# Kernel optimization log

Measured on AMD Instinct MI355X. Metric: run time of the kernel, lower is better.

Reference implementation:

```python
import jax, jax.numpy as jnp
import numpy as np

H, W, S, B = 256, 256, 16, 8  # dim=(H,W); S hardcoded in forward; B = 1 + events[-1,-1]
N = 4_000_000


def _shift2d(a, dy, dx):
    """Replicates F.pad(a, (pad(dx) + pad(dy)))[:H,:W] where pad(n)=(n,0) if n>=0 else (0,-n).
    Positive diff shifts content right/down and zero-fills; negative diff is a no-op
    (right/bottom padding followed by top-left crop is identity)."""
    sy = jnp.maximum(dy, 0)
    sx = jnp.maximum(dx, 0)
    a = jnp.roll(a, shift=(sy, sx), axis=(0, 1))
    row = jnp.arange(a.shape[0])[:, None]
    col = jnp.arange(a.shape[1])[None, :]
    return jnp.where((row >= sy) & (col >= sx), a, 0.0)


def setup_inputs():
    key = jax.random.key(0)
    k1, k2, k3, k4 = jax.random.split(key, 4)
    x = jax.random.randint(k1, (N,), 0, W).astype(jnp.float32)
    y = jax.random.randint(k2, (N,), 0, H).astype(jnp.float32)
    t = jax.random.uniform(k3, (N,), minval=1e-3, maxval=1.0)
    p = (jax.random.randint(k4, (N,), 0, 2) * 2 - 1).astype(jnp.float32)
    b = jnp.repeat(jnp.arange(B, dtype=jnp.float32), N // B)  # sorted so events[-1,-1]==B-1
    events = jnp.stack([x, y, t, p, b], axis=1)
    return {"events": events}


def _forward(events):
    x = events[:, 0]
    y = events[:, 1]
    t = events[:, 2]
    bi = events[:, 4].astype(jnp.int32)

    # per-batch time normalization: t /= max(t) within each sample
    t_max = jax.ops.segment_max(t, bi, num_segments=B)
    t = t / t_max[bi]

    xi = x.astype(jnp.int32)
    yi = y.astype(jnp.int32)

    # container: per-pixel event count histogram, (B,H,W)
    idx_c = xi + W * yi + W * H * bi
    container = jnp.zeros(B * H * W, jnp.int32).at[idx_c].add(1).reshape(B, H, W)

    # time_segment[e] = number of thresholds i/S (i=1..S-1) with t >= i/S
    thr = jnp.arange(1, S, dtype=t.dtype) / S
    ts = jnp.searchsorted(thr, t, side='right').astype(jnp.int32)

    # combiner accumulates the segment index itself (as in the torch code)
    idx_cb = xi + W * yi + W * H * ts + W * H * S * bi
    combiner = jnp.zeros(B * S * H * W, jnp.int32).at[idx_cb].add(ts)
    combiner = combiner.reshape(B, S, H, W).astype(jnp.float32)

    # per-(batch, segment) event counts and x/y centroids
    seg = bi * S + ts
    cnt = jax.ops.segment_sum(jnp.ones_like(t), seg, num_segments=B * S).reshape(B, S)
    xm = jax.ops.segment_sum(x, seg, num_segments=B * S).reshape(B, S) / cnt
    ym = jax.ops.segment_sum(y, seg, num_segments=B * S).reshape(B, S) / cnt

    # mean-shift alignment + accumulation of the S segment images
    combined = []
    for b_ in range(B):
        segment = combiner[b_, 0]
        x_mean = xm[b_, 0]
        y_mean = ym[b_, 0]
        pts = cnt[b_, 0]  # note: never updated in the original code
        for i in range(1, S):
            cond = cnt[b_, i] > pts
            tmp = jnp.where(cond, segment, combiner[b_, i])
            base = jnp.where(cond, combiner[b_, i], segment)
            dx = jnp.floor(jnp.where(cond, xm[b_, i] - x_mean, x_mean - xm[b_, i])).astype(jnp.int32)
            dy = jnp.floor(jnp.where(cond, ym[b_, i] - y_mean, y_mean - ym[b_, i])).astype(jnp.int32)
            x_mean = jnp.where(cond, xm[b_, i], x_mean)
            y_mean = jnp.where(cond, ym[b_, i], y_mean)
            segment = base + _shift2d(tmp, dy, dx)
        combined.append(jax.nn.relu(segment - S))
    combined_img = jnp.stack(combined)  # (B,H,W)

    # half-resolution count + mean-timestamp voxel grids
    hw4 = (H // 2) * (W // 2)
    idx_ct = xi // 2 + (W // 2) * (yi // 2) + (W * H * bi) // 4
    counter = jnp.zeros(B * hw4, jnp.int32).at[idx_ct].add(1).astype(jnp.float32)
    divider = jnp.where(counter == 0, 1.0, counter)
    timer = jnp.zeros(B * hw4, jnp.float32).at[idx_ct].add(t) / divider
    counter = counter.reshape(B, H // 2, W // 2)
    timer = timer.reshape(B, H // 2, W // 2)

    # 2x2 difference pooling of the count image
    dyv = container[:, ::2] - container[:, 1::2]
    dyv = (dyv[:, :, ::2] + dyv[:, :, 1::2]).astype(jnp.float32)
    dxv = container[:, :, ::2] - container[:, :, 1::2]
    dxv = (dxv[:, 1::2] + dxv[:, ::2]).astype(jnp.float32)

    # F.interpolate(scale_factor=0.5, mode='nearest') == ::2 subsampling for even H,W
    combined_half = combined_img[:, ::2, ::2]

    return jnp.stack([dxv, dyv, timer, counter, combined_half], axis=1)  # (B,5,H/2,W/2)


def reference(events):
    return _forward(events)
```

## Files before the change

### kernel.cpp

```cpp
#include <hip/hip_runtime.h>

#define SS 16
#define BB 8
#define CHUNKS 32

#define OFF_CNT    0
#define OFF_XS     512
#define OFF_YS     1024
#define OFF_BMAX   1536
#define OFF_P4REP  5632
#define OFF_CMREP  (5632 + 16777216)
#define OFF_XYREC  (5632 + 16777216 + 4194304)
#define OFF_TARR   (5632 + 16777216 + 4194304 + 8000000)
#define OFF_TSREC  (5632 + 16777216 + 4194304 + 8000000 + 16000000)


__global__ void k_prep(const float4* __restrict__ ev4, int nq, unsigned* __restrict__ bmax,
                       uint2* __restrict__ xyrec, float4* __restrict__ tarr,
                       int* __restrict__ cnt, int* __restrict__ xs, int* __restrict__ ys) {
    if (blockIdx.x == 0 && threadIdx.x < BB * SS) {
        cnt[threadIdx.x] = 0; xs[threadIdx.x] = 0; ys[threadIdx.x] = 0;
    }
    int bb = blockIdx.x >> 7;
    long base = (long)bb * nq;
    unsigned m = 0;
    for (int q = (blockIdx.x & 127) * blockDim.x + threadIdx.x; q < nq; q += 128 * blockDim.x) {
        const float4* p = ev4 + (base + q) * 5;
        float4 f0 = p[0], f1 = p[1], f2 = p[2], f3 = p[3], f4 = p[4];
        unsigned xy0 = (unsigned)(int)f0.x | ((unsigned)(int)f0.y << 8)
                     | ((unsigned)(int)f1.y << 16) | ((unsigned)(int)f1.z << 24);
        unsigned xy1 = (unsigned)(int)f2.z | ((unsigned)(int)f2.w << 8)
                     | ((unsigned)(int)f3.w << 16) | ((unsigned)(int)f4.x << 24);
        xyrec[base + q] = make_uint2(xy0, xy1);
        tarr[base + q]  = make_float4(f0.z, f1.w, f3.x, f4.y);
        unsigned t0 = __float_as_uint(f0.z), t1 = __float_as_uint(f1.w);
        unsigned t2 = __float_as_uint(f3.x), t3 = __float_as_uint(f4.y);
        unsigned a = t0 > t1 ? t0 : t1;
        unsigned b2 = t2 > t3 ? t2 : t3;
        a = a > b2 ? a : b2;
        m = m > a ? m : a;
    }
    #pragma unroll
    for (int off = 32; off; off >>= 1) {
        unsigned o = (unsigned)__shfl_xor((int)m, off, 64);
        m = m > o ? m : o;
    }
    __shared__ unsigned sm;
    if (threadIdx.x == 0) sm = 0;
    __syncthreads();
    if ((threadIdx.x & 63) == 0) atomicMax(&sm, m);
    __syncthreads();
    if (threadIdx.x == 0) bmax[blockIdx.x] = sm;
}

__global__ void __launch_bounds__(1024, 8)
k_main(const uint2* __restrict__ xyrec, const float4* __restrict__ tarr, int nq,
       const unsigned* __restrict__ bmax,
       unsigned* __restrict__ p4rep, unsigned short* __restrict__ tsrec,
       int* __restrict__ cnt, int* __restrict__ xs, int* __restrict__ ys) {
    __shared__ unsigned p4s[16384];
    __shared__ unsigned long long stat[SS * 16];
    __shared__ unsigned stmax;
    int bb = blockIdx.x >> 5;
    int ch = blockIdx.x & 31;
    if (threadIdx.x == 0) stmax = 0u;
    if (threadIdx.x < SS * 16) stat[threadIdx.x] = 0ull;
    {
        uint4 z = make_uint4(0u, 0u, 0u, 0u);
        uint4* p4 = (uint4*)p4s;
        for (int i = threadIdx.x; i < 4096; i += 1024) p4[i] = z;
    }
    __syncthreads();
    if (threadIdx.x < 128) atomicMax(&stmax, bmax[bb * 128 + threadIdx.x]);
    __syncthreads();
    float tm = __uint_as_float(stmax);
    long base = (long)bb * nq;
    int slot = threadIdx.x & 15;
    for (int q = ch * 1024 + threadIdx.x; q < nq; q += CHUNKS * 1024) {
        uint2 xy = xyrec[base + q];
        float4 t4 = tarr[base + q];
        float T[4] = { t4.x, t4.y, t4.z, t4.w };
        unsigned XY[4] = { xy.x & 0xFFFFu, xy.x >> 16, xy.y & 0xFFFFu, xy.y >> 16 };
        unsigned tsn = 0;
        #pragma unroll
        for (int k = 0; k < 4; k++) {
            int xi = (int)(XY[k] & 255u), yi = (int)(XY[k] >> 8);
            float tn = __fdiv_rn(T[k], tm);
            int ts = (int)(tn * 16.0f);
            if (ts > 15) ts = 15;
            unsigned qfix = __float2uint_rn(tn * 256.0f);
            unsigned v = qfix | (1u << 14)
                | (((unsigned)(xi & 1) ^ 1u) << 20)
                | (((unsigned)(yi & 1) ^ 1u) << 26);
            atomicAdd(&p4s[((yi >> 1) << 7) + (xi >> 1)], v);
            atomicAdd(&stat[ts * 16 + slot], 1ull | ((unsigned long long)xi << 20)
                                                  | ((unsigned long long)yi << 42));
            tsn |= (unsigned)ts << (4 * k);
        }
        tsrec[base + q] = (unsigned short)tsn;
    }
    __syncthreads();
    {
        uint4* src = (uint4*)p4s;
        uint4* dst = (uint4*)(p4rep + (long)blockIdx.x * 16384);
        for (int i = threadIdx.x; i < 4096; i += 1024) dst[i] = src[i];
    }
    if (threadIdx.x < SS) {
        unsigned long long v = 0ull;
        #pragma unroll
        for (int s = 0; s < 16; s++) v += stat[threadIdx.x * 16 + s];
        if (v) {
            int g = bb * SS + threadIdx.x;
            atomicAdd(&cnt[g], (int)(v & 0xFFFFF));
            atomicAdd(&xs[g],  (int)((v >> 20) & 0x3FFFFF));
            atomicAdd(&ys[g],  (int)(v >> 42));
        }
    }
}

__global__ void __launch_bounds__(1024, 8)
k_comb(const uint2* __restrict__ xyrec, const unsigned short* __restrict__ tsrec, int nq,
       const int* __restrict__ cnt, const int* __restrict__ xs, const int* __restrict__ ys,
       const unsigned* __restrict__ p4rep,
       unsigned* __restrict__ cmrep32, float* __restrict__ out) {
    __shared__ int combs[16384];
    __shared__ double xm[SS], ym[SS];
    __shared__ int cs[SS], ssy[SS], ssx[SS];
    int bb = blockIdx.x >> 5;
    int ch = blockIdx.x & 31;
    {
        int4 z = make_int4(0, 0, 0, 0);
        int4* cb = (int4*)combs;
        for (int i = threadIdx.x; i < 4096; i += 1024) cb[i] = z;
    }
    if (threadIdx.x < SS) {
        int g = bb * SS + threadIdx.x;
        int cc = cnt[g];
        cs[threadIdx.x] = cc;
        xm[threadIdx.x] = (double)xs[g] / (double)cc;
        ym[threadIdx.x] = (double)ys[g] / (double)cc;
    }
    __syncthreads();
    if (threadIdx.x == 0) {
        double x_mean = xm[0], y_mean = ym[0];
        int c0 = cs[0];
        int sy[SS], sx[SS];
        for (int k = 0; k < SS; k++) { sy[k] = 0; sx[k] = 0; }
        for (int k = 1; k < SS; k++) {
            bool cond = cs[k] > c0;
            double ddx = cond ? (xm[k] - x_mean) : (x_mean - xm[k]);
            double ddy = cond ? (ym[k] - y_mean) : (y_mean - ym[k]);
            int dx = (int)floor(ddx);
            int dy = (int)floor(ddy);
            int px = dx > 0 ? dx : 0;
            int py = dy > 0 ? dy : 0;
            if (cond) {
                for (int j = 0; j < k; j++) { sy[j] += py; sx[j] += px; }
                x_mean = xm[k]; y_mean = ym[k];
            } else {
                sy[k] = py; sx[k] = px;
            }
        }
        for (int k = 0; k < SS; k++) { ssy[k] = sy[k]; ssx[k] = sx[k]; }
    }
    __syncthreads();
    long base = (long)bb * nq;
    for (int q = ch * 1024 + threadIdx.x; q < nq; q += CHUNKS * 1024) {
        uint2 xy = xyrec[base + q];
        unsigned tsn = tsrec[base + q];
        unsigned XY[4] = { xy.x & 0xFFFFu, xy.x >> 16, xy.y & 0xFFFFu, xy.y >> 16 };
        #pragma unroll
        for (int k = 0; k < 4; k++) {
            int ts = (int)((tsn >> (4 * k)) & 15u);
            if (ts) {
                int yy = (int)(XY[k] >> 8) + ssy[ts];
                int xx = (int)(XY[k] & 255u) + ssx[ts];
                if (yy < 256 && xx < 256 && !((yy | xx) & 1))
                    atomicAdd(&combs[((yy >> 1) << 7) + (xx >> 1)], ts);
            }
        }
    }
    __syncthreads();
    {
        unsigned* dst = cmrep32 + (long)blockIdx.x * 4096;
        int4* cb = (int4*)combs;
        for (int i = threadIdx.x; i < 4096; i += 1024) {
            int4 c = cb[i];
            dst[i] = (unsigned)c.x | ((unsigned)c.y << 8)
                   | ((unsigned)c.z << 16) | ((unsigned)c.w << 24);
        }
    }
    if (threadIdx.x < 512) {
        int lin = blockIdx.x * 512 + threadIdx.x;
        int hp = lin & 16383;
        int b  = lin >> 14;
        long rb = (long)b * CHUNKS * 16384 + hp;
        unsigned tfix = 0; int c = 0, Ex = 0, Ey = 0;
        #pragma unroll 8
        for (int r = 0; r < CHUNKS; r++) {
            unsigned v = p4rep[rb + (long)r * 16384];
            tfix += v & 0x3FFFu;
            c    += (int)((v >> 14) & 63u);
            Ex   += (int)((v >> 20) & 63u);
            Ey   += (int)(v >> 26);
        }
        float tsum = (float)tfix * (1.0f / 256.0f);
        float ctr = (float)c;
        int obase = (b * 5) << 14;
        out[obase             + hp] = (float)(2 * Ex - c);
        out[obase +     16384 + hp] = (float)(2 * Ey - c);
        out[obase + 2 * 16384 + hp] = tsum / (c == 0 ? 1.0f : ctr);
        out[obase + 3 * 16384 + hp] = ctr;
    }
}

__global__ void k_out(const unsigned* __restrict__ cmrep32, float* __restrict__ out) {
    int lin4 = blockIdx.x * blockDim.x + threadIdx.x;
    int hp4 = lin4 & 4095;
    int b   = lin4 >> 12;
    long rb = (long)b * CHUNKS * 4096 + hp4;
    unsigned accA = 0, accB = 0;
    #pragma unroll 8
    for (int r = 0; r < CHUNKS; r++) {
        unsigned v = cmrep32[rb + (long)r * 4096];
        accA += v & 0x00FF00FFu;
        accB += (v >> 8) & 0x00FF00FFu;
    }
    float c0 = (float)(accA & 0xFFFFu) - 16.0f;
    float c1 = (float)(accB & 0xFFFFu) - 16.0f;
    float c2 = (float)(accA >> 16) - 16.0f;
    float c3 = (float)(accB >> 16) - 16.0f;
    float4 o;
    o.x = c0 < 0.0f ? 0.0f : c0;
    o.y = c1 < 0.0f ? 0.0f : c1;
    o.z = c2 < 0.0f ? 0.0f : c2;
    o.w = c3 < 0.0f ? 0.0f : c3;
    ((float4*)out)[(((b * 5 + 4) << 14) >> 2) + hp4] = o;
}

extern "C" void kernel_launch(void* const* d_in, const int* in_sizes, int n_in,
                              void* d_out, int out_size, void* d_ws, size_t ws_size,
                              hipStream_t stream) {
    const float4* ev4 = (const float4*)d_in[0];
    int n  = in_sizes[0] / 5;
    int nb = n / BB;
    int nq = nb / 4;
    char* ws = (char*)d_ws;
    int*      cnt     = (int*)     (ws + OFF_CNT);
    int*      xs      = (int*)     (ws + OFF_XS);
    int*      ys      = (int*)     (ws + OFF_YS);
    unsigned* bmax    = (unsigned*)(ws + OFF_BMAX);
    unsigned* p4rep   = (unsigned*)(ws + OFF_P4REP);
    unsigned* cmrep32 = (unsigned*)(ws + OFF_CMREP);
    uint2*    xyrec   = (uint2*)   (ws + OFF_XYREC);
    float4*   tarr    = (float4*)  (ws + OFF_TARR);
    unsigned short* tsrec = (unsigned short*)(ws + OFF_TSREC);

    hipLaunchKernelGGL(k_prep, dim3(1024), dim3(256),  0, stream, ev4, nq, bmax,
                       xyrec, tarr, cnt, xs, ys);
    hipLaunchKernelGGL(k_main, dim3(256),  dim3(1024), 0, stream, xyrec, tarr, nq,
                       bmax, p4rep, tsrec, cnt, xs, ys);
    hipLaunchKernelGGL(k_comb, dim3(256),  dim3(1024), 0, stream, xyrec, tsrec, nq,
                       cnt, xs, ys, p4rep, cmrep32, (float*)d_out);
    hipLaunchKernelGGL(k_out,  dim3(32),   dim3(1024), 0, stream,
                       cmrep32, (float*)d_out);
}
```

Baseline: 138.4 us.

## Drop compacted intermediate arrays and re-read raw events in each pass

```diff
diff --git a/kernel.cpp b/kernel.cpp
--- a/kernel.cpp
+++ b/kernel.cpp
@@ -8,15 +8,11 @@
 #define OFF_XS     512
 #define OFF_YS     1024
 #define OFF_BMAX   1536
-#define OFF_P4REP  5632
-#define OFF_CMREP  (5632 + 16777216)
-#define OFF_XYREC  (5632 + 16777216 + 4194304)
-#define OFF_TARR   (5632 + 16777216 + 4194304 + 8000000)
-#define OFF_TSREC  (5632 + 16777216 + 4194304 + 8000000 + 16000000)
-
-
-__global__ void k_prep(const float4* __restrict__ ev4, int nq, unsigned* __restrict__ bmax,
-                       uint2* __restrict__ xyrec, float4* __restrict__ tarr,
+#define OFF_P4REP  8192
+#define OFF_CMREP  (8192 + 16777216)
+
+
+__global__ void k_tmax(const float4* __restrict__ ev4, int nq, unsigned* __restrict__ bmax,
                        int* __restrict__ cnt, int* __restrict__ xs, int* __restrict__ ys) {
     if (blockIdx.x == 0 && threadIdx.x < BB * SS) {
         cnt[threadIdx.x] = 0; xs[threadIdx.x] = 0; ys[threadIdx.x] = 0;
@@ -26,13 +22,7 @@
     unsigned m = 0;
     for (int q = (blockIdx.x & 127) * blockDim.x + threadIdx.x; q < nq; q += 128 * blockDim.x) {
         const float4* p = ev4 + (base + q) * 5;
-        float4 f0 = p[0], f1 = p[1], f2 = p[2], f3 = p[3], f4 = p[4];
-        unsigned xy0 = (unsigned)(int)f0.x | ((unsigned)(int)f0.y << 8)
-                     | ((unsigned)(int)f1.y << 16) | ((unsigned)(int)f1.z << 24);
-        unsigned xy1 = (unsigned)(int)f2.z | ((unsigned)(int)f2.w << 8)
-                     | ((unsigned)(int)f3.w << 16) | ((unsigned)(int)f4.x << 24);
-        xyrec[base + q] = make_uint2(xy0, xy1);
-        tarr[base + q]  = make_float4(f0.z, f1.w, f3.x, f4.y);
+        float4 f0 = p[0], f1 = p[1], f3 = p[3], f4 = p[4];
         unsigned t0 = __float_as_uint(f0.z), t1 = __float_as_uint(f1.w);
         unsigned t2 = __float_as_uint(f3.x), t3 = __float_as_uint(f4.y);
         unsigned a = t0 > t1 ? t0 : t1;
@@ -54,9 +44,8 @@
 }
 
 __global__ void __launch_bounds__(1024, 8)
-k_main(const uint2* __restrict__ xyrec, const float4* __restrict__ tarr, int nq,
-       const unsigned* __restrict__ bmax,
-       unsigned* __restrict__ p4rep, unsigned short* __restrict__ tsrec,
+k_main(const float4* __restrict__ ev4, int nq, const unsigned* __restrict__ bmax,
+       unsigned* __restrict__ p4rep,
        int* __restrict__ cnt, int* __restrict__ xs, int* __restrict__ ys) {
     __shared__ unsigned p4s[16384];
     __shared__ unsigned long long stat[SS * 16];
@@ -77,14 +66,14 @@
     long base = (long)bb * nq;
     int slot = threadIdx.x & 15;
     for (int q = ch * 1024 + threadIdx.x; q < nq; q += CHUNKS * 1024) {
-        uint2 xy = xyrec[base + q];
-        float4 t4 = tarr[base + q];
-        float T[4] = { t4.x, t4.y, t4.z, t4.w };
-        unsigned XY[4] = { xy.x & 0xFFFFu, xy.x >> 16, xy.y & 0xFFFFu, xy.y >> 16 };
-        unsigned tsn = 0;
+        const float4* p = ev4 + (base + q) * 5;
+        float4 f0 = p[0], f1 = p[1], f2 = p[2], f3 = p[3], f4 = p[4];
+        int X[4] = { (int)f0.x, (int)f1.y, (int)f2.z, (int)f3.w };
+        int Y[4] = { (int)f0.y, (int)f1.z, (int)f2.w, (int)f4.x };
+        float T[4] = { f0.z, f1.w, f3.x, f4.y };
         #pragma unroll
         for (int k = 0; k < 4; k++) {
-            int xi = (int)(XY[k] & 255u), yi = (int)(XY[k] >> 8);
+            int xi = X[k], yi = Y[k];
             float tn = __fdiv_rn(T[k], tm);
             int ts = (int)(tn * 16.0f);
             if (ts > 15) ts = 15;
@@ -95,9 +84,7 @@
             atomicAdd(&p4s[((yi >> 1) << 7) + (xi >> 1)], v);
             atomicAdd(&stat[ts * 16 + slot], 1ull | ((unsigned long long)xi << 20)
                                                   | ((unsigned long long)yi << 42));
-            tsn |= (unsigned)ts << (4 * k);
-        }
-        tsrec[base + q] = (unsigned short)tsn;
+        }
     }
     __syncthreads();
     {
@@ -119,15 +106,17 @@
 }
 
 __global__ void __launch_bounds__(1024, 8)
-k_comb(const uint2* __restrict__ xyrec, const unsigned short* __restrict__ tsrec, int nq,
+k_comb(const float4* __restrict__ ev4, int nq, const unsigned* __restrict__ bmax,
        const int* __restrict__ cnt, const int* __restrict__ xs, const int* __restrict__ ys,
        const unsigned* __restrict__ p4rep,
        unsigned* __restrict__ cmrep32, float* __restrict__ out) {
     __shared__ int combs[16384];
+    __shared__ unsigned stmax;
     __shared__ double xm[SS], ym[SS];
     __shared__ int cs[SS], ssy[SS], ssx[SS];
     int bb = blockIdx.x >> 5;
     int ch = blockIdx.x & 31;
+    if (threadIdx.x == 0) stmax = 0u;
     {
         int4 z = make_int4(0, 0, 0, 0);
         int4* cb = (int4*)combs;
@@ -141,6 +130,7 @@
         ym[threadIdx.x] = (double)ys[g] / (double)cc;
     }
     __syncthreads();
+    if (threadIdx.x < 128) atomicMax(&stmax, bmax[bb * 128 + threadIdx.x]);
     if (threadIdx.x == 0) {
         double x_mean = xm[0], y_mean = ym[0];
         int c0 = cs[0];
@@ -164,17 +154,22 @@
         for (int k = 0; k < SS; k++) { ssy[k] = sy[k]; ssx[k] = sx[k]; }
     }
     __syncthreads();
+    float tm = __uint_as_float(stmax);
     long base = (long)bb * nq;
     for (int q = ch * 1024 + threadIdx.x; q < nq; q += CHUNKS * 1024) {
-        uint2 xy = xyrec[base + q];
-        unsigned tsn = tsrec[base + q];
-        unsigned XY[4] = { xy.x & 0xFFFFu, xy.x >> 16, xy.y & 0xFFFFu, xy.y >> 16 };
+        const float4* p = ev4 + (base + q) * 5;
+        float4 f0 = p[0], f1 = p[1], f2 = p[2], f3 = p[3], f4 = p[4];
+        int X[4] = { (int)f0.x, (int)f1.y, (int)f2.z, (int)f3.w };
+        int Y[4] = { (int)f0.y, (int)f1.z, (int)f2.w, (int)f4.x };
+        float T[4] = { f0.z, f1.w, f3.x, f4.y };
         #pragma unroll
         for (int k = 0; k < 4; k++) {
-            int ts = (int)((tsn >> (4 * k)) & 15u);
+            float tn = __fdiv_rn(T[k], tm);
+            int ts = (int)(tn * 16.0f);
+            if (ts > 15) ts = 15;
             if (ts) {
-                int yy = (int)(XY[k] >> 8) + ssy[ts];
-                int xx = (int)(XY[k] & 255u) + ssx[ts];
+                int yy = Y[k] + ssy[ts];
+                int xx = X[k] + ssx[ts];
                 if (yy < 256 && xx < 256 && !((yy | xx) & 1))
                     atomicAdd(&combs[((yy >> 1) << 7) + (xx >> 1)], ts);
             }
@@ -252,15 +247,12 @@
     unsigned* bmax    = (unsigned*)(ws + OFF_BMAX);
     unsigned* p4rep   = (unsigned*)(ws + OFF_P4REP);
     unsigned* cmrep32 = (unsigned*)(ws + OFF_CMREP);
-    uint2*    xyrec   = (uint2*)   (ws + OFF_XYREC);
-    float4*   tarr    = (float4*)  (ws + OFF_TARR);
-    unsigned short* tsrec = (unsigned short*)(ws + OFF_TSREC);
-
-    hipLaunchKernelGGL(k_prep, dim3(1024), dim3(256),  0, stream, ev4, nq, bmax,
-                       xyrec, tarr, cnt, xs, ys);
-    hipLaunchKernelGGL(k_main, dim3(256),  dim3(1024), 0, stream, xyrec, tarr, nq,
-                       bmax, p4rep, tsrec, cnt, xs, ys);
-    hipLaunchKernelGGL(k_comb, dim3(256),  dim3(1024), 0, stream, xyrec, tsrec, nq,
+
+    hipLaunchKernelGGL(k_tmax, dim3(1024), dim3(256),  0, stream, ev4, nq, bmax,
+                       cnt, xs, ys);
+    hipLaunchKernelGGL(k_main, dim3(256),  dim3(1024), 0, stream, ev4, nq, bmax,
+                       p4rep, cnt, xs, ys);
+    hipLaunchKernelGGL(k_comb, dim3(256),  dim3(1024), 0, stream, ev4, nq, bmax,
                        cnt, xs, ys, p4rep, cmrep32, (float*)d_out);
     hipLaunchKernelGGL(k_out,  dim3(32),   dim3(1024), 0, stream,
                        cmrep32, (float*)d_out);
```

New measurement: 148.6 us. 7.3% more time.
